# Kernel tuning notes

Measured on AMD Instinct MI355X. Metric: run time of the kernel, lower is better.

The kernel has to match this reference:

```python
import jax, jax.numpy as jnp
import numpy as np

N, IN_F, OUT_F = 4096, 512, 16
HID = [128, 64, 32]
H = 4  # num_head
LRELU_SLOPE = 0.2
BN_EPS = 1e-5
NEG_INF = -1e9


def _gat(x, adj_mask, W, a_src, a_dst, heads, f_out):
    n = x.shape[0]
    h = (x @ W).reshape(n, heads, f_out)              # [N,H,F]
    es = jnp.einsum('nhf,hf->hn', h, a_src)           # [H,N]
    ed = jnp.einsum('nhf,hf->hn', h, a_dst)           # [H,N]
    e = jax.nn.leaky_relu(es[:, :, None] + ed[:, None, :], LRELU_SLOPE)  # [H,N,N]
    e = jnp.where(adj_mask[None], e, NEG_INF)
    attn = jax.nn.softmax(e, axis=-1)                 # masked softmax over neighbors
    out = jnp.einsum('hij,jhf->ihf', attn, h)         # [N,H,F]
    return out.reshape(n, heads * f_out)


def _bn_elu(x, gamma, beta):
    mu = jnp.mean(x, axis=0)
    var = jnp.var(x, axis=0)
    xhat = (x - mu) * jax.lax.rsqrt(var + BN_EPS)
    return jax.nn.elu(xhat * gamma + beta)


def setup_inputs() -> dict:
    key = jax.random.key(0)
    ks = jax.random.split(key, 14)
    s = lambda fin: 1.0 / np.sqrt(fin)
    x = jax.random.normal(ks[0], (N, IN_F), jnp.float32)
    adj = jax.random.randint(ks[1], (N, N), 0, 2, jnp.int32)
    W1 = jax.random.normal(ks[2], (IN_F, H * HID[0]), jnp.float32) * s(IN_F)
    a1s = jax.random.normal(ks[3], (H, HID[0]), jnp.float32) * s(HID[0])
    a1d = jax.random.normal(ks[4], (H, HID[0]), jnp.float32) * s(HID[0])
    lw1 = jax.random.normal(ks[5], (H * HID[0], HID[1]), jnp.float32) * s(H * HID[0])
    lb1 = jnp.zeros((HID[1],), jnp.float32)
    g1 = jnp.ones((HID[1],), jnp.float32)
    be1 = jnp.zeros((HID[1],), jnp.float32)
    W2 = jax.random.normal(ks[6], (HID[1], H * HID[2]), jnp.float32) * s(HID[1])
    a2s = jax.random.normal(ks[7], (H, HID[2]), jnp.float32) * s(HID[2])
    a2d = jax.random.normal(ks[8], (H, HID[2]), jnp.float32) * s(HID[2])
    lw2 = jax.random.normal(ks[9], (H * HID[2], OUT_F), jnp.float32) * s(H * HID[2])
    lb2 = jnp.zeros((OUT_F,), jnp.float32)
    g2 = jnp.ones((OUT_F,), jnp.float32)
    be2 = jnp.zeros((OUT_F,), jnp.float32)
    return dict(x=x, adj=adj, W1=W1, a1s=a1s, a1d=a1d, lw1=lw1, lb1=lb1, g1=g1, be1=be1,
                W2=W2, a2s=a2s, a2d=a2d, lw2=lw2, lb2=lb2, g2=g2, be2=be2)


def reference(x, adj, W1, a1s, a1d, lw1, lb1, g1, be1, W2, a2s, a2d, lw2, lb2, g2, be2):
    adj_mask = adj > 0
    x1 = _gat(x, adj_mask, W1, a1s, a1d, H, HID[0])        # [N, H*128]
    x2 = _bn_elu(x1 @ lw1 + lb1, g1, be1)                  # [N, 64]
    x3 = _gat(x2, adj_mask, W2, a2s, a2d, H, HID[2])       # [N, H*32]
    out = _bn_elu(x3 @ lw2 + lb2, g2, be2)                 # [N, 16]
    return out
```

## Files before the change

kernel.cpp:

```cpp
#include <hip/hip_runtime.h>
#include <hip/hip_bf16.h>
#include <stdint.h>

#define NN 4096
#define H4 4

typedef __hip_bfloat16 bf16;
typedef unsigned short ushort_t;
typedef unsigned long long ull_t;
typedef __attribute__((ext_vector_type(4))) float f32x4;
typedef __attribute__((ext_vector_type(8))) short s16x8;

__device__ __forceinline__ ushort_t f2bf(float f) {
  unsigned u = __float_as_uint(f);
  return (ushort_t)((u + 0x7fff + ((u >> 16) & 1)) >> 16);
}
__device__ __forceinline__ float bf2f(ushort_t h) {
  return __uint_as_float((unsigned)h << 16);
}
__device__ __forceinline__ short2 pkbf(float a, float b) {
  union { __hip_bfloat162 h; short2 s; } u;
  u.h = __float22bfloat162_rn(make_float2(a, b));
  return u.s;
}
__device__ __forceinline__ s16x8 as_s16x8(uint4 v) {
  union { uint4 u; s16x8 s; } c; c.u = v; return c.s;
}

__global__ __launch_bounds__(256) void k_mask(const int* __restrict__ adj,
                                              ull_t* __restrict__ mask) {
  int row = blockIdx.x, tid = threadIdx.x;
  int lane = tid & 63, wv = tid >> 6;
  const int* arow = adj + (size_t)row * NN;
  for (int c = 0; c < NN; c += 256) {
    int col = c + wv * 64 + lane;
    ull_t b = __ballot(arow[col] != 0);
    if (lane == 0) mask[row * 64 + (c >> 6) + wv] = b;
  }
}

__global__ __launch_bounds__(256) void k_gemm(const float* __restrict__ A,
                                              const float* __restrict__ B,
                                              const float* __restrict__ bias,
                                              float* __restrict__ C, int M, int K, int Nc) {
  __shared__ float As[16][68];
  __shared__ float Bs[16][68];
  int tid = threadIdx.x;
  int tx = tid & 15, ty = tid >> 4;
  int mBase = blockIdx.y * 64, nBase = blockIdx.x * 64;
  float acc[4][4] = {};
  for (int k0 = 0; k0 < K; k0 += 16) {
#pragma unroll
    for (int l = 0; l < 4; ++l) {
      int idx = l * 256 + tid;
      int m = idx >> 4, k = idx & 15;
      As[k][m] = A[(size_t)(mBase + m) * K + (k0 + k)];
    }
#pragma unroll
    for (int l = 0; l < 4; ++l) {
      int idx = l * 256 + tid;
      int k = idx >> 6, n = idx & 63;
      int gn = nBase + n;
      Bs[k][n] = (gn < Nc) ? B[(size_t)(k0 + k) * Nc + gn] : 0.f;
    }
    __syncthreads();
#pragma unroll
    for (int k = 0; k < 16; ++k) {
      float4 a = *(const float4*)&As[k][ty * 4];
      float4 b = *(const float4*)&Bs[k][tx * 4];
      float av[4] = {a.x, a.y, a.z, a.w};
      float bv[4] = {b.x, b.y, b.z, b.w};
#pragma unroll
      for (int r = 0; r < 4; ++r)
#pragma unroll
        for (int c = 0; c < 4; ++c) acc[r][c] += av[r] * bv[c];
    }
    __syncthreads();
  }
#pragma unroll
  for (int r = 0; r < 4; ++r) {
    int gm = mBase + ty * 4 + r;
#pragma unroll
    for (int c = 0; c < 4; ++c) {
      int gn = nBase + tx * 4 + c;
      if (gn < Nc) {
        float v = acc[r][c];
        if (bias) v += bias[gn];
        C[(size_t)gm * Nc + gn] = v;
      }
    }
  }
}

#define APLANE (4096 * 512)
template <int KK, int NC>
__device__ __forceinline__ void packW_dev(const float* __restrict__ W,
                                          ushort_t* __restrict__ pk, int tau, int lane) {
  constexpr int KS = KK / 32;
  constexpr int T = (NC / 16) * KS;
  constexpr int PL = T * 512;
  if (tau >= T) return;
  int q = lane >> 4, nn = lane & 15;
  int ct = tau / KS, ks = tau % KS;
  ushort_t hi[8], lo[8];
#pragma unroll
  for (int u = 0; u < 8; ++u) {
    float v = W[(size_t)(ks * 32 + q * 8 + u) * NC + ct * 16 + nn];
    hi[u] = f2bf(v);
    lo[u] = f2bf(v - bf2f(hi[u]));
  }
  size_t idx = ((size_t)(ct * KS + ks) * 64 + lane) * 8;
  *(uint4*)&pk[idx] = *(uint4*)hi;
  *(uint4*)&pk[PL + idx] = *(uint4*)lo;
}

__global__ __launch_bounds__(256) void k_packP(const float* __restrict__ x,
                                               const float* __restrict__ W1,
                                               const float* __restrict__ lw1,
                                               const float* __restrict__ lw2,
                                               ushort_t* __restrict__ pkA,
                                               ushort_t* __restrict__ pkW1,
                                               ushort_t* __restrict__ pkLW1,
                                               ushort_t* __restrict__ pkLW2) {
  int b = blockIdx.x, t = threadIdx.x;
  int w = t >> 6, lane = t & 63;
  if (b < 1024) {
    int q = lane >> 4, nn = lane & 15;
    int tau = b * 4 + w;
    int mt = tau >> 4, ks = tau & 15;
    const float* src = &x[(size_t)(mt * 16 + nn) * 512 + ks * 32 + q * 8];
    float4 v0 = *(const float4*)src;
    float4 v1 = *(const float4*)(src + 4);
    float vv[8] = {v0.x, v0.y, v0.z, v0.w, v1.x, v1.y, v1.z, v1.w};
    ushort_t hi[8], lo[8];
#pragma unroll
    for (int u = 0; u < 8; ++u) {
      hi[u] = f2bf(vv[u]);
      lo[u] = f2bf(vv[u] - bf2f(hi[u]));
    }
    size_t idx = ((size_t)(mt * 16 + ks) * 64 + lane) * 8;
    *(uint4*)&pkA[idx] = *(uint4*)hi;
    *(uint4*)&pkA[APLANE + idx] = *(uint4*)lo;
  } else if (b < 1152) {
    packW_dev<512, 512>(W1, pkW1, (b - 1024) * 4 + w, lane);
  } else if (b < 1168) {
    packW_dev<512, 64>(lw1, pkLW1, (b - 1152) * 4 + w, lane);
  } else {
    packW_dev<128, 16>(lw2, pkLW2, (b - 1168) * 4 + w, lane);
  }
}

__global__ __launch_bounds__(256, 1) void k_mm1(const uint4* __restrict__ pkA,
                                                const uint4* __restrict__ pkW,
                                                float* __restrict__ h1) {
  constexpr int APL4 = APLANE / 8;
  constexpr int WPL4 = (512 / 16) * (512 / 32) * 64;
  int t = threadIdx.x;
  int w = t >> 6, lane = t & 63;
  int q = lane >> 4, nn = lane & 15;
  int mt0 = blockIdx.x * 4 + (w & 1) * 2;
  int ct0 = blockIdx.y * 8 + (w >> 1) * 4;
  f32x4 acc[2][4];
#pragma unroll
  for (int rt = 0; rt < 2; ++rt)
#pragma unroll
    for (int c = 0; c < 4; ++c)
#pragma unroll
      for (int k = 0; k < 4; ++k) acc[rt][c][k] = 0.f;
#pragma unroll
  for (int ks = 0; ks < 16; ++ks) {
    int ia0 = (mt0 * 16 + ks) * 64 + lane;
    int ia1 = ((mt0 + 1) * 16 + ks) * 64 + lane;
    uint4 ah0 = pkA[ia0], ah1 = pkA[ia1];
    uint4 al0 = pkA[APL4 + ia0], al1 = pkA[APL4 + ia1];
    uint4 bh[4], bl[4];
#pragma unroll
    for (int c = 0; c < 4; ++c) {
      int ib = ((ct0 + c) * 16 + ks) * 64 + lane;
      bh[c] = pkW[ib];
      bl[c] = pkW[WPL4 + ib];
    }
#pragma unroll
    for (int c = 0; c < 4; ++c) {
      acc[0][c] = __builtin_amdgcn_mfma_f32_16x16x32_bf16(as_s16x8(ah0), as_s16x8(bh[c]), acc[0][c], 0, 0, 0);
      acc[0][c] = __builtin_amdgcn_mfma_f32_16x16x32_bf16(as_s16x8(ah0), as_s16x8(bl[c]), acc[0][c], 0, 0, 0);
      acc[0][c] = __builtin_amdgcn_mfma_f32_16x16x32_bf16(as_s16x8(al0), as_s16x8(bh[c]), acc[0][c], 0, 0, 0);
      acc[1][c] = __builtin_amdgcn_mfma_f32_16x16x32_bf16(as_s16x8(ah1), as_s16x8(bh[c]), acc[1][c], 0, 0, 0);
      acc[1][c] = __builtin_amdgcn_mfma_f32_16x16x32_bf16(as_s16x8(ah1), as_s16x8(bl[c]), acc[1][c], 0, 0, 0);
      acc[1][c] = __builtin_amdgcn_mfma_f32_16x16x32_bf16(as_s16x8(al1), as_s16x8(bh[c]), acc[1][c], 0, 0, 0);
    }
  }
  int rowB = blockIdx.x * 64 + (w & 1) * 32;
#pragma unroll
  for (int rt = 0; rt < 2; ++rt)
#pragma unroll
    for (int c = 0; c < 4; ++c)
#pragma unroll
      for (int reg = 0; reg < 4; ++reg) {
        int gi = rowB + rt * 16 + q * 4 + reg;
        h1[(size_t)gi * 512 + (ct0 + c) * 16 + nn] = acc[rt][c][reg];
      }
}

template <int F, int TB>
__global__ __launch_bounds__(TB) void k_pack(const float* __restrict__ h,
                                             ushort_t* __restrict__ pk) {
  constexpr int CTW = TB / 64;
  int t = threadIdx.x;
  int lane = t & 63, ctw = t >> 6;
  int q = lane >> 4, nn = lane & 15;
  int ks = blockIdx.x, hd = blockIdx.y;
#pragma unroll
  for (int ct = ctw; ct < F / 16; ct += CTW) {
    ushort_t v[8];
#pragma unroll
    for (int u = 0; u < 8; ++u)
      v[u] = f2bf(h[(size_t)(ks * 32 + q * 8 + u) * (H4 * F) + hd * F + ct * 16 + nn]);
    *(uint4*)&pk[((((size_t)hd * (F / 16) + ct) * (NN / 32) + ks) * 64 + lane) * 8] =
        *(uint4*)v;
  }
}

template <int F>
__global__ __launch_bounds__(256) void k_scores(const float* __restrict__ h,
                                                const float* __restrict__ a_s,
                                                const float* __restrict__ a_d,
                                                float* __restrict__ Tt, float* __restrict__ E1,
                                                float* __restrict__ E2, float* __restrict__ D1,
                                                float* __restrict__ D2) {
  int idx = blockIdx.x * 256 + threadIdx.x;
  if (idx >= NN * H4) return;
  int n = idx >> 2, hd = idx & 3;
  const float* hp = h + (size_t)n * (H4 * F) + hd * F;
  const float* sp = a_s + hd * F;
  const float* dp = a_d + hd * F;
  float ss = 0.f, sd = 0.f;
#pragma unroll 4
  for (int f = 0; f < F; ++f) {
    float v = hp[f];
    ss += v * sp[f];
    sd += v * dp[f];
  }
  ss = fminf(fmaxf(ss, -30.f), 30.f);
  sd = fminf(fmaxf(sd, -30.f), 30.f);
  int o = hd * NN + n;
  Tt[o] = __expf(-ss);
  E1[o] = __expf(ss);
  E2[o] = __expf(0.2f * ss);
  D1[o] = __expf(sd);
  D2[o] = __expf(0.2f * sd);
}

__device__ __forceinline__ s16x8 build_af(float E1i, float E2i, float Ti, unsigned byt,
                                          float4 d1a, float4 d1b, float4 d2a, float4 d2b,
                                          float& rs) {
  float d1[8] = {d1a.x, d1a.y, d1a.z, d1a.w, d1b.x, d1b.y, d1b.z, d1b.w};
  float d2[8] = {d2a.x, d2a.y, d2a.z, d2a.w, d2b.x, d2b.y, d2b.z, d2b.w};
  union { s16x8 v; short2 p[4]; } A;
#pragma unroll
  for (int tp = 0; tp < 4; ++tp) {
    int k0 = 2 * tp, k1 = 2 * tp + 1;
    bool p0 = d1[k0] > Ti;
    float u0 = (p0 ? E1i : E2i) * (p0 ? d1[k0] : d2[k0]);
    u0 = (byt & (1u << k0)) ? u0 : 0.f;
    bool p1 = d1[k1] > Ti;
    float u1 = (p1 ? E1i : E2i) * (p1 ? d1[k1] : d2[k1]);
    u1 = (byt & (1u << k1)) ? u1 : 0.f;
    rs += u0 + u1;
    A.p[tp] = pkbf(u0, u1);
  }
  return A.v;
}

template <int F, int OUTM>
__global__ __launch_bounds__(256, 2) void k_agg_mfma(
    const uint4* __restrict__ pk, const float* __restrict__ Tt,
    const float* __restrict__ E1, const float* __restrict__ E2,
    const float* __restrict__ D1, const float* __restrict__ D2,
    const ull_t* __restrict__ mask, ushort_t* __restrict__ pkOut) {
  constexpr int CT = F / 16;
  constexpr int KSO = (H4 * F) / 32;
  constexpr int OPL = NN * H4 * F;
  __shared__ float red[2 * 32 * F];
  __shared__ float rsred[32 * 4];
  int t = threadIdx.x;
  int w = t >> 6, lane = t & 63;
  int q = lane >> 4, nn = lane & 15;
  int hd = blockIdx.y;
  int rowBase = blockIdx.x * 32;
  int jBase = w * (NN / 4);
  int ia0 = rowBase + nn, ia1 = rowBase + 16 + nn;
  float E1i0 = E1[hd * NN + ia0], E2i0 = E2[hd * NN + ia0], Ti0 = Tt[hd * NN + ia0];
  float E1i1 = E1[hd * NN + ia1], E2i1 = E2[hd * NN + ia1], Ti1 = Tt[hd * NN + ia1];
  const ull_t* mk0p = mask + (size_t)ia0 * 64;
  const ull_t* mk1p = mask + (size_t)ia1 * 64;
  const float* d1h = D1 + hd * NN;
  const float* d2h = D2 + hd * NN;

  f32x4 acc[2][CT];
#pragma unroll
  for (int rt = 0; rt < 2; ++rt)
#pragma unroll
    for (int cc = 0; cc < CT; ++cc)
#pragma unroll
      for (int k = 0; k < 4; ++k) acc[rt][cc][k] = 0.f;
  float rs0 = 0.f, rs1 = 0.f;

  for (int jc = 0; jc < NN / 4 / 64; ++jc) {
    int j0 = jBase + jc * 64;
    int ks0 = j0 >> 5;
    uint4 bv[2][CT];
#pragma unroll
    for (int s = 0; s < 2; ++s)
#pragma unroll
      for (int cc = 0; cc < CT; ++cc)
        bv[s][cc] = pk[(size_t)((hd * CT + cc) * (NN / 32) + ks0 + s) * 64 + lane];
    ull_t mk0 = mk0p[j0 >> 6], mk1 = mk1p[j0 >> 6];
    float4 d1a = *(const float4*)&d1h[j0 + q * 8];
    float4 d1b = *(const float4*)&d1h[j0 + q * 8 + 4];
    float4 d2a = *(const float4*)&d2h[j0 + q * 8];
    float4 d2b = *(const float4*)&d2h[j0 + q * 8 + 4];
    float4 d1c = *(const float4*)&d1h[j0 + 32 + q * 8];
    float4 d1d = *(const float4*)&d1h[j0 + 32 + q * 8 + 4];
    float4 d2c = *(const float4*)&d2h[j0 + 32 + q * 8];
    float4 d2d = *(const float4*)&d2h[j0 + 32 + q * 8 + 4];
    s16x8 a00 = build_af(E1i0, E2i0, Ti0, (unsigned)(mk0 >> (q * 8)) & 0xffu, d1a, d1b, d2a, d2b, rs0);
    s16x8 a01 = build_af(E1i0, E2i0, Ti0, (unsigned)(mk0 >> (32 + q * 8)) & 0xffu, d1c, d1d, d2c, d2d, rs0);
    s16x8 a10 = build_af(E1i1, E2i1, Ti1, (unsigned)(mk1 >> (q * 8)) & 0xffu, d1a, d1b, d2a, d2b, rs1);
    s16x8 a11 = build_af(E1i1, E2i1, Ti1, (unsigned)(mk1 >> (32 + q * 8)) & 0xffu, d1c, d1d, d2c, d2d, rs1);
#pragma unroll
    for (int cc = 0; cc < CT; ++cc)
      acc[0][cc] = __builtin_amdgcn_mfma_f32_16x16x32_bf16(a00, as_s16x8(bv[0][cc]), acc[0][cc], 0, 0, 0);
#pragma unroll
    for (int cc = 0; cc < CT; ++cc)
      acc[0][cc] = __builtin_amdgcn_mfma_f32_16x16x32_bf16(a01, as_s16x8(bv[1][cc]), acc[0][cc], 0, 0, 0);
#pragma unroll
    for (int cc = 0; cc < CT; ++cc)
      acc[1][cc] = __builtin_amdgcn_mfma_f32_16x16x32_bf16(a10, as_s16x8(bv[0][cc]), acc[1][cc], 0, 0, 0);
#pragma unroll
    for (int cc = 0; cc < CT; ++cc)
      acc[1][cc] = __builtin_amdgcn_mfma_f32_16x16x32_bf16(a11, as_s16x8(bv[1][cc]), acc[1][cc], 0, 0, 0);
  }

  rs0 += __shfl_xor(rs0, 16, 64); rs0 += __shfl_xor(rs0, 32, 64);
  rs1 += __shfl_xor(rs1, 16, 64); rs1 += __shfl_xor(rs1, 32, 64);
  if (q == 0) {
    rsred[nn * 4 + w] = rs0;
    rsred[(16 + nn) * 4 + w] = rs1;
  }

#define IDX(rt, cc, reg) ((rt * 16 + q * 4 + reg) * F + cc * 16 + nn)
  if (w == 1 || w == 3) {
    int base = (w >> 1) * 32 * F;
#pragma unroll
    for (int rt = 0; rt < 2; ++rt)
#pragma unroll
      for (int cc = 0; cc < CT; ++cc)
#pragma unroll
        for (int reg = 0; reg < 4; ++reg) red[base + IDX(rt, cc, reg)] = acc[rt][cc][reg];
  }
  __syncthreads();
  if (w == 0 || w == 2) {
    int base = (w >> 1) * 32 * F;
#pragma unroll
    for (int rt = 0; rt < 2; ++rt)
#pragma unroll
      for (int cc = 0; cc < CT; ++cc)
#pragma unroll
        for (int reg = 0; reg < 4; ++reg) acc[rt][cc][reg] += red[base + IDX(rt, cc, reg)];
  }
  if (w == 2) {
#pragma unroll
    for (int rt = 0; rt < 2; ++rt)
#pragma unroll
      for (int cc = 0; cc < CT; ++cc)
#pragma unroll
        for (int reg = 0; reg < 4; ++reg) red[32 * F + IDX(rt, cc, reg)] = acc[rt][cc][reg];
  }
  __syncthreads();
  if (w == 0) {
    float rinv[2][4];
#pragma unroll
    for (int rt = 0; rt < 2; ++rt)
#pragma unroll
      for (int reg = 0; reg < 4; ++reg) {
        int row = rt * 16 + q * 4 + reg;
        float4 rv = *(float4*)&rsred[row * 4];
        float s = (rv.x + rv.y) + (rv.z + rv.w);
        rinv[rt][reg] = (s > 0.f) ? 1.f / s : 0.f;
      }
#pragma unroll
    for (int rt = 0; rt < 2; ++rt)
#pragma unroll
      for (int cc = 0; cc < CT; ++cc)
#pragma unroll
        for (int reg = 0; reg < 4; ++reg) {
          float v = (acc[rt][cc][reg] + red[32 * F + IDX(rt, cc, reg)]) * rinv[rt][reg];
          int gi = rowBase + rt * 16 + q * 4 + reg;
          int c = hd * F + cc * 16 + nn;
          int mt = gi >> 4, rowin = gi & 15;
          int ks = c >> 5, qp = (c >> 3) & 3, u = c & 7;
          size_t idx = (((size_t)mt * KSO + ks) * 64 + qp * 16 + rowin) * 8 + u;
          ushort_t hi = f2bf(v);
          pkOut[idx] = hi;
          if (OUTM == 1) pkOut[OPL + idx] = f2bf(v - bf2f(hi));
        }
  }
#undef IDX
}

__global__ __launch_bounds__(256) void k_mm2(const uint4* __restrict__ pkX,
                                             const uint4* __restrict__ pkW,
                                             const float* __restrict__ bias,
                                             float* __restrict__ y) {
  constexpr int WPL4 = 4 * 16 * 64;
  __shared__ float red[2 * 16 * 64];
  int t = threadIdx.x;
  int w = t >> 6, lane = t & 63;
  int q = lane >> 4, nn = lane & 15;
  int mt = blockIdx.x * 2 + (w & 1);
  int kh = w >> 1;
  f32x4 acc[4];
#pragma unroll
  for (int c = 0; c < 4; ++c)
#pragma unroll
    for (int k = 0; k < 4; ++k) acc[c][k] = 0.f;
#pragma unroll
  for (int k8 = 0; k8 < 8; ++k8) {
    int ks = kh * 8 + k8;
    uint4 a = pkX[(mt * 16 + ks) * 64 + lane];
#pragma unroll
    for (int c = 0; c < 4; ++c) {
      uint4 bh = pkW[(c * 16 + ks) * 64 + lane];
      uint4 bl = pkW[WPL4 + (c * 16 + ks) * 64 + lane];
      acc[c] = __builtin_amdgcn_mfma_f32_16x16x32_bf16(as_s16x8(a), as_s16x8(bh), acc[c], 0, 0, 0);
      acc[c] = __builtin_amdgcn_mfma_f32_16x16x32_bf16(as_s16x8(a), as_s16x8(bl), acc[c], 0, 0, 0);
    }
  }
  int base = (w & 1) * 1024;
  if (kh == 1) {
#pragma unroll
    for (int c = 0; c < 4; ++c)
#pragma unroll
      for (int reg = 0; reg < 4; ++reg)
        red[base + (q * 4 + reg) * 64 + c * 16 + nn] = acc[c][reg];
  }
  __syncthreads();
  if (kh == 0) {
#pragma unroll
    for (int c = 0; c < 4; ++c)
#pragma unroll
      for (int reg = 0; reg < 4; ++reg) {
        float v = acc[c][reg] + red[base + (q * 4 + reg) * 64 + c * 16 + nn] + bias[c * 16 + nn];
        y[(size_t)(mt * 16 + q * 4 + reg) * 64 + c * 16 + nn] = v;
      }
  }
}

__global__ __launch_bounds__(256) void k_mm4(const uint4* __restrict__ pkX,
                                             const uint4* __restrict__ pkW,
                                             const float* __restrict__ bias,
                                             float* __restrict__ y) {
  constexpr int XPL4 = 256 * 4 * 64;
  constexpr int WPL4 = 1 * 4 * 64;
  int t = threadIdx.x;
  int w = t >> 6, lane = t & 63;
  int q = lane >> 4, nn = lane & 15;
  int mt = blockIdx.x * 4 + w;
  f32x4 acc;
#pragma unroll
  for (int k = 0; k < 4; ++k) acc[k] = 0.f;
#pragma unroll
  for (int ks = 0; ks < 4; ++ks) {
    uint4 ah = pkX[(mt * 4 + ks) * 64 + lane];
    uint4 al = pkX[XPL4 + (mt * 4 + ks) * 64 + lane];
    uint4 bh = pkW[ks * 64 + lane];
    uint4 bl = pkW[WPL4 + ks * 64 + lane];
    acc = __builtin_amdgcn_mfma_f32_16x16x32_bf16(as_s16x8(ah), as_s16x8(bh), acc, 0, 0, 0);
    acc = __builtin_amdgcn_mfma_f32_16x16x32_bf16(as_s16x8(ah), as_s16x8(bl), acc, 0, 0, 0);
    acc = __builtin_amdgcn_mfma_f32_16x16x32_bf16(as_s16x8(al), as_s16x8(bh), acc, 0, 0, 0);
  }
  float b = bias[nn];
#pragma unroll
  for (int reg = 0; reg < 4; ++reg)
    y[(size_t)(mt * 16 + q * 4 + reg) * 16 + nn] = acc[reg] + b;
}

__global__ __launch_bounds__(256) void k_bn_col(const float* __restrict__ y,
                                                const float* __restrict__ gamma,
                                                const float* __restrict__ beta,
                                                float* __restrict__ o, int C) {
  int c = blockIdx.x, tid = threadIdx.x;
  float s = 0.f, s2 = 0.f;
  for (int r = tid; r < NN; r += 256) {
    float v = y[(size_t)r * C + c];
    s += v;
    s2 += v * v;
  }
  __shared__ float sh[256], sh2[256];
  __shared__ float smu, srs;
  sh[tid] = s; sh2[tid] = s2;
  __syncthreads();
  for (int off = 128; off; off >>= 1) {
    if (tid < off) { sh[tid] += sh[tid + off]; sh2[tid] += sh2[tid + off]; }
    __syncthreads();
  }
  if (tid == 0) {
    float mu = sh[0] * (1.f / NN);
    float var = sh2[0] * (1.f / NN) - mu * mu;
    smu = mu;
    srs = rsqrtf(fmaxf(var, 0.f) + 1e-5f);
  }
  __syncthreads();
  float mu = smu, rstd = srs, g = gamma[c], b = beta[c];
  for (int r = tid; r < NN; r += 256) {
    float v = (y[(size_t)r * C + c] - mu) * rstd * g + b;
    v = v > 0.f ? v : (__expf(v) - 1.f);
    o[(size_t)r * C + c] = v;
  }
}

extern "C" void kernel_launch(void* const* d_in, const int* in_sizes, int n_in,
                              void* d_out, int out_size, void* d_ws, size_t ws_size,
                              hipStream_t stream) {
  (void)in_sizes; (void)n_in; (void)out_size; (void)ws_size;
  const float* x   = (const float*)d_in[0];
  const int*   adj = (const int*)d_in[1];
  const float* W1  = (const float*)d_in[2];
  const float* a1s = (const float*)d_in[3];
  const float* a1d = (const float*)d_in[4];
  const float* lw1 = (const float*)d_in[5];
  const float* lb1 = (const float*)d_in[6];
  const float* g1  = (const float*)d_in[7];
  const float* be1 = (const float*)d_in[8];
  const float* W2  = (const float*)d_in[9];
  const float* a2s = (const float*)d_in[10];
  const float* a2d = (const float*)d_in[11];
  const float* lw2 = (const float*)d_in[12];
  const float* lb2 = (const float*)d_in[13];
  const float* g2  = (const float*)d_in[14];
  const float* be2 = (const float*)d_in[15];
  float* out = (float*)d_out;

  char* w = (char*)d_ws;
  const size_t MB = 1u << 20;
  ull_t*    mask  = (ull_t*)(w + 0);
  ushort_t* pkA   = (ushort_t*)(w + 2 * MB);
  ushort_t* pkW1  = (ushort_t*)(w + 10 * MB);
  float*    h1    = (float*)(w + 11 * MB);
  ushort_t* pk1   = (ushort_t*)(w + 19 * MB);
  float*    T1    = (float*)(w + 23 * MB);
  float*    E1a   = T1 + 16384;
  float*    E2a   = E1a + 16384;
  float*    D1a   = E2a + 16384;
  float*    D2a   = D1a + 16384;
  ushort_t* pkX1  = (ushort_t*)(w + 24 * MB);
  ushort_t* pkLW1 = (ushort_t*)(w + 28 * MB);
  float*    y1    = (float*)(w + 29 * MB);
  float*    x2    = (float*)(w + 30 * MB);
  float*    h2    = (float*)(w + 31 * MB);
  ushort_t* pk2   = (ushort_t*)(w + 33 * MB);
  float*    T2    = (float*)(w + 34 * MB);
  float*    E1b   = T2 + 16384;
  float*    E2b   = E1b + 16384;
  float*    D1b   = E2b + 16384;
  float*    D2b   = D1b + 16384;
  ushort_t* pkX3  = (ushort_t*)(w + 35 * MB);
  ushort_t* pkLW2 = (ushort_t*)(w + 37 * MB);
  float*    y2    = (float*)(w + 37 * MB + 131072);

  k_mask<<<NN, 256, 0, stream>>>(adj, mask);
  k_packP<<<1169, 256, 0, stream>>>(x, W1, lw1, lw2, pkA, pkW1, pkLW1, pkLW2);

  k_mm1<<<dim3(64, 4), 256, 0, stream>>>((const uint4*)pkA, (const uint4*)pkW1, h1);
  k_pack<128, 256><<<dim3(NN / 32, H4), 256, 0, stream>>>(h1, pk1);
  k_scores<128><<<(NN * H4) / 256, 256, 0, stream>>>(h1, a1s, a1d, T1, E1a, E2a, D1a, D2a);
  k_agg_mfma<128, 0><<<dim3(NN / 32, H4), 256, 0, stream>>>((const uint4*)pk1, T1, E1a, E2a,
                                                            D1a, D2a, mask, pkX1);

  k_mm2<<<128, 256, 0, stream>>>((const uint4*)pkX1, (const uint4*)pkLW1, lb1, y1);
  k_bn_col<<<64, 256, 0, stream>>>(y1, g1, be1, x2, 64);

  k_gemm<<<dim3(2, 64), 256, 0, stream>>>(x2, W2, nullptr, h2, NN, 64, 128);
  k_pack<32, 128><<<dim3(NN / 32, H4), 128, 0, stream>>>(h2, pk2);
  k_scores<32><<<(NN * H4) / 256, 256, 0, stream>>>(h2, a2s, a2d, T2, E1b, E2b, D1b, D2b);
  k_agg_mfma<32, 1><<<dim3(NN / 32, H4), 256, 0, stream>>>((const uint4*)pk2, T2, E1b, E2b,
                                                           D1b, D2b, mask, pkX3);

  k_mm4<<<64, 256, 0, stream>>>((const uint4*)pkX3, (const uint4*)pkLW2, lb2, y2);
  k_bn_col<<<16, 256, 0, stream>>>(y2, g2, be2, out, 16);
}
```

Baseline: 294.0 us.

## Build attention weights in packed fp16 and fold row sums into MFMA

Score exponentials are stored as scaled fp16, and attention weights are formed with packed fp16 multiply and max (max(E1*D1, E2*D2) is exp of the leaky relu), replacing the per-element compare and select in fp32. Row sums come from an extra MFMA against a ones vector instead of scalar accumulation and shuffles. The aggregation MFMAs switch from bf16 to fp16 and the reduction buffer is padded. The intent is to cut VALU work in the attention build loop. In exchange, scores are clamped to ±8 and fp16 range and precision limits could affect accuracy.

```diff
diff --git a/kernel.cpp b/kernel.cpp
--- a/kernel.cpp
+++ b/kernel.cpp
@@ -10,6 +10,8 @@
 typedef unsigned long long ull_t;
 typedef __attribute__((ext_vector_type(4))) float f32x4;
 typedef __attribute__((ext_vector_type(8))) short s16x8;
+typedef __attribute__((ext_vector_type(2))) _Float16 h16x2;
+typedef __attribute__((ext_vector_type(8))) _Float16 h16x8;
 
 __device__ __forceinline__ ushort_t f2bf(float f) {
   unsigned u = __float_as_uint(f);
@@ -18,13 +20,25 @@
 __device__ __forceinline__ float bf2f(ushort_t h) {
   return __uint_as_float((unsigned)h << 16);
 }
-__device__ __forceinline__ short2 pkbf(float a, float b) {
-  union { __hip_bfloat162 h; short2 s; } u;
-  u.h = __float22bfloat162_rn(make_float2(a, b));
-  return u.s;
-}
 __device__ __forceinline__ s16x8 as_s16x8(uint4 v) {
   union { uint4 u; s16x8 s; } c; c.u = v; return c.s;
+}
+__device__ __forceinline__ unsigned pkmul(unsigned a, unsigned b) {
+  union { unsigned u; h16x2 v; } A, B, R;
+  A.u = a; B.u = b;
+  R.v = A.v * B.v;
+  return R.u;
+}
+__device__ __forceinline__ unsigned pkmax(unsigned a, unsigned b) {
+  union { unsigned u; h16x2 v; } A, B, R;
+  A.u = a; B.u = b;
+  R.v = __builtin_elementwise_max(A.v, B.v);
+  return R.u;
+}
+__device__ __forceinline__ ushort_t f2h(float f) {
+  union { _Float16 h; ushort_t s; } c;
+  c.h = (_Float16)f;
+  return c.s;
 }
 
 __global__ __launch_bounds__(256) void k_mask(const int* __restrict__ adj,
@@ -215,7 +229,7 @@
     ushort_t v[8];
 #pragma unroll
     for (int u = 0; u < 8; ++u)
-      v[u] = f2bf(h[(size_t)(ks * 32 + q * 8 + u) * (H4 * F) + hd * F + ct * 16 + nn]);
+      v[u] = f2h(h[(size_t)(ks * 32 + q * 8 + u) * (H4 * F) + hd * F + ct * 16 + nn]);
     *(uint4*)&pk[((((size_t)hd * (F / 16) + ct) * (NN / 32) + ks) * 64 + lane) * 8] =
         *(uint4*)v;
   }
@@ -225,9 +239,10 @@
 __global__ __launch_bounds__(256) void k_scores(const float* __restrict__ h,
                                                 const float* __restrict__ a_s,
                                                 const float* __restrict__ a_d,
-                                                float* __restrict__ Tt, float* __restrict__ E1,
-                                                float* __restrict__ E2, float* __restrict__ D1,
-                                                float* __restrict__ D2) {
+                                                ushort_t* __restrict__ E1s,
+                                                ushort_t* __restrict__ E2s,
+                                                ushort_t* __restrict__ D1s,
+                                                ushort_t* __restrict__ D2s) {
   int idx = blockIdx.x * 256 + threadIdx.x;
   if (idx >= NN * H4) return;
   int n = idx >> 2, hd = idx & 3;
@@ -241,48 +256,44 @@
     ss += v * sp[f];
     sd += v * dp[f];
   }
-  ss = fminf(fmaxf(ss, -30.f), 30.f);
-  sd = fminf(fmaxf(sd, -30.f), 30.f);
+  ss = fminf(fmaxf(ss, -8.f), 8.f);
+  sd = fminf(fmaxf(sd, -8.f), 8.f);
   int o = hd * NN + n;
-  Tt[o] = __expf(-ss);
-  E1[o] = __expf(ss);
-  E2[o] = __expf(0.2f * ss);
-  D1[o] = __expf(sd);
-  D2[o] = __expf(0.2f * sd);
-}
-
-__device__ __forceinline__ s16x8 build_af(float E1i, float E2i, float Ti, unsigned byt,
-                                          float4 d1a, float4 d1b, float4 d2a, float4 d2b,
-                                          float& rs) {
-  float d1[8] = {d1a.x, d1a.y, d1a.z, d1a.w, d1b.x, d1b.y, d1b.z, d1b.w};
-  float d2[8] = {d2a.x, d2a.y, d2a.z, d2a.w, d2b.x, d2b.y, d2b.z, d2b.w};
-  union { s16x8 v; short2 p[4]; } A;
+  E1s[o] = f2h(__expf(ss) * 0.0625f);
+  E2s[o] = f2h(__expf(0.2f * ss) * 0.0625f);
+  D1s[o] = f2h(__expf(sd) * 0.0625f);
+  D2s[o] = f2h(__expf(0.2f * sd) * 0.0625f);
+}
+
+__device__ __forceinline__ void build_af(unsigned E1pk, unsigned E2pk, unsigned byt,
+                                         uint4 d1, uint4 d2, unsigned out[4]) {
+  unsigned d1v[4] = {d1.x, d1.y, d1.z, d1.w};
+  unsigned d2v[4] = {d2.x, d2.y, d2.z, d2.w};
 #pragma unroll
   for (int tp = 0; tp < 4; ++tp) {
-    int k0 = 2 * tp, k1 = 2 * tp + 1;
-    bool p0 = d1[k0] > Ti;
-    float u0 = (p0 ? E1i : E2i) * (p0 ? d1[k0] : d2[k0]);
-    u0 = (byt & (1u << k0)) ? u0 : 0.f;
-    bool p1 = d1[k1] > Ti;
-    float u1 = (p1 ? E1i : E2i) * (p1 ? d1[k1] : d2[k1]);
-    u1 = (byt & (1u << k1)) ? u1 : 0.f;
-    rs += u0 + u1;
-    A.p[tp] = pkbf(u0, u1);
-  }
-  return A.v;
+    unsigned u = pkmax(pkmul(E1pk, d1v[tp]), pkmul(E2pk, d2v[tp]));
+    int mlo = (int)(byt << (31 - 2 * tp)) >> 31;
+    int mhi = (int)(byt << (30 - 2 * tp)) >> 31;
+    out[tp] = u & (((unsigned)mlo & 0xFFFFu) | ((unsigned)mhi << 16));
+  }
+}
+__device__ __forceinline__ h16x8 as_h16x8(const unsigned w[4]) {
+  union { unsigned u[4]; h16x8 v; } c;
+  c.u[0] = w[0]; c.u[1] = w[1]; c.u[2] = w[2]; c.u[3] = w[3];
+  return c.v;
 }
 
 template <int F, int OUTM>
 __global__ __launch_bounds__(256, 2) void k_agg_mfma(
-    const uint4* __restrict__ pk, const float* __restrict__ Tt,
-    const float* __restrict__ E1, const float* __restrict__ E2,
-    const float* __restrict__ D1, const float* __restrict__ D2,
-    const ull_t* __restrict__ mask, ushort_t* __restrict__ pkOut) {
+    const uint4* __restrict__ pk, const ushort_t* __restrict__ E1s,
+    const ushort_t* __restrict__ E2s, const ushort_t* __restrict__ D1s,
+    const ushort_t* __restrict__ D2s, const ull_t* __restrict__ mask,
+    ushort_t* __restrict__ pkOut) {
   constexpr int CT = F / 16;
+  constexpr int RW = F + 16;
   constexpr int KSO = (H4 * F) / 32;
   constexpr int OPL = NN * H4 * F;
-  __shared__ float red[2 * 32 * F];
-  __shared__ float rsred[32 * 4];
+  __shared__ float red[2 * 32 * RW];
   int t = threadIdx.x;
   int w = t >> 6, lane = t & 63;
   int q = lane >> 4, nn = lane & 15;
@@ -290,22 +301,28 @@
   int rowBase = blockIdx.x * 32;
   int jBase = w * (NN / 4);
   int ia0 = rowBase + nn, ia1 = rowBase + 16 + nn;
-  float E1i0 = E1[hd * NN + ia0], E2i0 = E2[hd * NN + ia0], Ti0 = Tt[hd * NN + ia0];
-  float E1i1 = E1[hd * NN + ia1], E2i1 = E2[hd * NN + ia1], Ti1 = Tt[hd * NN + ia1];
+  unsigned E1p0 = (unsigned)E1s[hd * NN + ia0] * 0x00010001u;
+  unsigned E2p0 = (unsigned)E2s[hd * NN + ia0] * 0x00010001u;
+  unsigned E1p1 = (unsigned)E1s[hd * NN + ia1] * 0x00010001u;
+  unsigned E2p1 = (unsigned)E2s[hd * NN + ia1] * 0x00010001u;
   const ull_t* mk0p = mask + (size_t)ia0 * 64;
   const ull_t* mk1p = mask + (size_t)ia1 * 64;
-  const float* d1h = D1 + hd * NN;
-  const float* d2h = D2 + hd * NN;
-
-  f32x4 acc[2][CT];
+  const ushort_t* d1h = D1s + hd * NN;
+  const ushort_t* d2h = D2s + hd * NN;
+
+  h16x8 ones;
+#pragma unroll
+  for (int k = 0; k < 8; ++k) ones[k] = (_Float16)1.0f;
+
+  f32x4 acc[2][CT + 1];
 #pragma unroll
   for (int rt = 0; rt < 2; ++rt)
 #pragma unroll
-    for (int cc = 0; cc < CT; ++cc)
+    for (int cc = 0; cc <= CT; ++cc)
 #pragma unroll
       for (int k = 0; k < 4; ++k) acc[rt][cc][k] = 0.f;
-  float rs0 = 0.f, rs1 = 0.f;
-
+
+#pragma unroll 2
   for (int jc = 0; jc < NN / 4 / 64; ++jc) {
     int j0 = jBase + jc * 64;
     int ks0 = j0 >> 5;
@@ -316,56 +333,49 @@
       for (int cc = 0; cc < CT; ++cc)
         bv[s][cc] = pk[(size_t)((hd * CT + cc) * (NN / 32) + ks0 + s) * 64 + lane];
     ull_t mk0 = mk0p[j0 >> 6], mk1 = mk1p[j0 >> 6];
-    float4 d1a = *(const float4*)&d1h[j0 + q * 8];
-    float4 d1b = *(const float4*)&d1h[j0 + q * 8 + 4];
-    float4 d2a = *(const float4*)&d2h[j0 + q * 8];
-    float4 d2b = *(const float4*)&d2h[j0 + q * 8 + 4];
-    float4 d1c = *(const float4*)&d1h[j0 + 32 + q * 8];
-    float4 d1d = *(const float4*)&d1h[j0 + 32 + q * 8 + 4];
-    float4 d2c = *(const float4*)&d2h[j0 + 32 + q * 8];
-    float4 d2d = *(const float4*)&d2h[j0 + 32 + q * 8 + 4];
-    s16x8 a00 = build_af(E1i0, E2i0, Ti0, (unsigned)(mk0 >> (q * 8)) & 0xffu, d1a, d1b, d2a, d2b, rs0);
-    s16x8 a01 = build_af(E1i0, E2i0, Ti0, (unsigned)(mk0 >> (32 + q * 8)) & 0xffu, d1c, d1d, d2c, d2d, rs0);
-    s16x8 a10 = build_af(E1i1, E2i1, Ti1, (unsigned)(mk1 >> (q * 8)) & 0xffu, d1a, d1b, d2a, d2b, rs1);
-    s16x8 a11 = build_af(E1i1, E2i1, Ti1, (unsigned)(mk1 >> (32 + q * 8)) & 0xffu, d1c, d1d, d2c, d2d, rs1);
-#pragma unroll
-    for (int cc = 0; cc < CT; ++cc)
-      acc[0][cc] = __builtin_amdgcn_mfma_f32_16x16x32_bf16(a00, as_s16x8(bv[0][cc]), acc[0][cc], 0, 0, 0);
-#pragma unroll
-    for (int cc = 0; cc < CT; ++cc)
-      acc[0][cc] = __builtin_amdgcn_mfma_f32_16x16x32_bf16(a01, as_s16x8(bv[1][cc]), acc[0][cc], 0, 0, 0);
-#pragma unroll
-    for (int cc = 0; cc < CT; ++cc)
-      acc[1][cc] = __builtin_amdgcn_mfma_f32_16x16x32_bf16(a10, as_s16x8(bv[0][cc]), acc[1][cc], 0, 0, 0);
-#pragma unroll
-    for (int cc = 0; cc < CT; ++cc)
-      acc[1][cc] = __builtin_amdgcn_mfma_f32_16x16x32_bf16(a11, as_s16x8(bv[1][cc]), acc[1][cc], 0, 0, 0);
-  }
-
-  rs0 += __shfl_xor(rs0, 16, 64); rs0 += __shfl_xor(rs0, 32, 64);
-  rs1 += __shfl_xor(rs1, 16, 64); rs1 += __shfl_xor(rs1, 32, 64);
-  if (q == 0) {
-    rsred[nn * 4 + w] = rs0;
-    rsred[(16 + nn) * 4 + w] = rs1;
-  }
-
-#define IDX(rt, cc, reg) ((rt * 16 + q * 4 + reg) * F + cc * 16 + nn)
+    uint4 d1a = *(const uint4*)&d1h[j0 + q * 8];
+    uint4 d2a = *(const uint4*)&d2h[j0 + q * 8];
+    uint4 d1b = *(const uint4*)&d1h[j0 + 32 + q * 8];
+    uint4 d2b = *(const uint4*)&d2h[j0 + 32 + q * 8];
+    unsigned a00[4], a01[4], a10[4], a11[4];
+    build_af(E1p0, E2p0, (unsigned)(mk0 >> (q * 8)) & 0xffu, d1a, d2a, a00);
+    build_af(E1p0, E2p0, (unsigned)(mk0 >> (32 + q * 8)) & 0xffu, d1b, d2b, a01);
+    build_af(E1p1, E2p1, (unsigned)(mk1 >> (q * 8)) & 0xffu, d1a, d2a, a10);
+    build_af(E1p1, E2p1, (unsigned)(mk1 >> (32 + q * 8)) & 0xffu, d1b, d2b, a11);
+    h16x8 A00 = as_h16x8(a00), A01 = as_h16x8(a01);
+    h16x8 A10 = as_h16x8(a10), A11 = as_h16x8(a11);
+#pragma unroll
+    for (int cc = 0; cc < CT; ++cc) {
+      union { uint4 u; h16x8 v; } b0, b1;
+      b0.u = bv[0][cc]; b1.u = bv[1][cc];
+      acc[0][cc] = __builtin_amdgcn_mfma_f32_16x16x32_f16(A00, b0.v, acc[0][cc], 0, 0, 0);
+      acc[0][cc] = __builtin_amdgcn_mfma_f32_16x16x32_f16(A01, b1.v, acc[0][cc], 0, 0, 0);
+      acc[1][cc] = __builtin_amdgcn_mfma_f32_16x16x32_f16(A10, b0.v, acc[1][cc], 0, 0, 0);
+      acc[1][cc] = __builtin_amdgcn_mfma_f32_16x16x32_f16(A11, b1.v, acc[1][cc], 0, 0, 0);
+    }
+    acc[0][CT] = __builtin_amdgcn_mfma_f32_16x16x32_f16(A00, ones, acc[0][CT], 0, 0, 0);
+    acc[0][CT] = __builtin_amdgcn_mfma_f32_16x16x32_f16(A01, ones, acc[0][CT], 0, 0, 0);
+    acc[1][CT] = __builtin_amdgcn_mfma_f32_16x16x32_f16(A10, ones, acc[1][CT], 0, 0, 0);
+    acc[1][CT] = __builtin_amdgcn_mfma_f32_16x16x32_f16(A11, ones, acc[1][CT], 0, 0, 0);
+  }
+
+#define IDX(rt, cc, reg) ((rt * 16 + q * 4 + reg) * RW + cc * 16 + nn)
   if (w == 1 || w == 3) {
-    int base = (w >> 1) * 32 * F;
+    int base = (w >> 1) * 32 * RW;
 #pragma unroll
     for (int rt = 0; rt < 2; ++rt)
 #pragma unroll
-      for (int cc = 0; cc < CT; ++cc)
+      for (int cc = 0; cc <= CT; ++cc)
 #pragma unroll
         for (int reg = 0; reg < 4; ++reg) red[base + IDX(rt, cc, reg)] = acc[rt][cc][reg];
   }
   __syncthreads();
   if (w == 0 || w == 2) {
-    int base = (w >> 1) * 32 * F;
+    int base = (w >> 1) * 32 * RW;
 #pragma unroll
     for (int rt = 0; rt < 2; ++rt)
 #pragma unroll
-      for (int cc = 0; cc < CT; ++cc)
+      for (int cc = 0; cc <= CT; ++cc)
 #pragma unroll
         for (int reg = 0; reg < 4; ++reg) acc[rt][cc][reg] += red[base + IDX(rt, cc, reg)];
   }
@@ -373,9 +383,9 @@
 #pragma unroll
     for (int rt = 0; rt < 2; ++rt)
 #pragma unroll
-      for (int cc = 0; cc < CT; ++cc)
-#pragma unroll
-        for (int reg = 0; reg < 4; ++reg) red[32 * F + IDX(rt, cc, reg)] = acc[rt][cc][reg];
+      for (int cc = 0; cc <= CT; ++cc)
+#pragma unroll
+        for (int reg = 0; reg < 4; ++reg) red[32 * RW + IDX(rt, cc, reg)] = acc[rt][cc][reg];
   }
   __syncthreads();
   if (w == 0) {
@@ -384,9 +394,7 @@
     for (int rt = 0; rt < 2; ++rt)
 #pragma unroll
       for (int reg = 0; reg < 4; ++reg) {
-        int row = rt * 16 + q * 4 + reg;
-        float4 rv = *(float4*)&rsred[row * 4];
-        float s = (rv.x + rv.y) + (rv.z + rv.w);
+        float s = acc[rt][CT][reg] + red[32 * RW + IDX(rt, CT, reg)];
         rinv[rt][reg] = (s > 0.f) ? 1.f / s : 0.f;
       }
 #pragma unroll
@@ -395,7 +403,7 @@
       for (int cc = 0; cc < CT; ++cc)
 #pragma unroll
         for (int reg = 0; reg < 4; ++reg) {
-          float v = (acc[rt][cc][reg] + red[32 * F + IDX(rt, cc, reg)]) * rinv[rt][reg];
+          float v = (acc[rt][cc][reg] + red[32 * RW + IDX(rt, cc, reg)]) * rinv[rt][reg];
           int gi = rowBase + rt * 16 + q * 4 + reg;
           int c = hd * F + cc * 16 + nn;
           int mt = gi >> 4, rowin = gi & 15;
@@ -549,22 +557,20 @@
   ushort_t* pkW1  = (ushort_t*)(w + 10 * MB);
   float*    h1    = (float*)(w + 11 * MB);
   ushort_t* pk1   = (ushort_t*)(w + 19 * MB);
-  float*    T1    = (float*)(w + 23 * MB);
-  float*    E1a   = T1 + 16384;
-  float*    E2a   = E1a + 16384;
-  float*    D1a   = E2a + 16384;
-  float*    D2a   = D1a + 16384;
+  ushort_t* E1a   = (ushort_t*)(w + 23 * MB);
+  ushort_t* E2a   = E1a + 16384;
+  ushort_t* D1a   = E2a + 16384;
+  ushort_t* D2a   = D1a + 16384;
   ushort_t* pkX1  = (ushort_t*)(w + 24 * MB);
   ushort_t* pkLW1 = (ushort_t*)(w + 28 * MB);
   float*    y1    = (float*)(w + 29 * MB);
   float*    x2    = (float*)(w + 30 * MB);
   float*    h2    = (float*)(w + 31 * MB);
   ushort_t* pk2   = (ushort_t*)(w + 33 * MB);
-  float*    T2    = (float*)(w + 34 * MB);
-  float*    E1b   = T2 + 16384;
-  float*    E2b   = E1b + 16384;
-  float*    D1b   = E2b + 16384;
-  float*    D2b   = D1b + 16384;
+  ushort_t* E1b   = (ushort_t*)(w + 34 * MB);
+  ushort_t* E2b   = E1b + 16384;
+  ushort_t* D1b   = E2b + 16384;
+  ushort_t* D2b   = D1b + 16384;
   ushort_t* pkX3  = (ushort_t*)(w + 35 * MB);
   ushort_t* pkLW2 = (ushort_t*)(w + 37 * MB);
   float*    y2    = (float*)(w + 37 * MB + 131072);
@@ -574,8 +580,8 @@
 
   k_mm1<<<dim3(64, 4), 256, 0, stream>>>((const uint4*)pkA, (const uint4*)pkW1, h1);
   k_pack<128, 256><<<dim3(NN / 32, H4), 256, 0, stream>>>(h1, pk1);
-  k_scores<128><<<(NN * H4) / 256, 256, 0, stream>>>(h1, a1s, a1d, T1, E1a, E2a, D1a, D2a);
-  k_agg_mfma<128, 0><<<dim3(NN / 32, H4), 256, 0, stream>>>((const uint4*)pk1, T1, E1a, E2a,
+  k_scores<128><<<(NN * H4) / 256, 256, 0, stream>>>(h1, a1s, a1d, E1a, E2a, D1a, D2a);
+  k_agg_mfma<128, 0><<<dim3(NN / 32, H4), 256, 0, stream>>>((const uint4*)pk1, E1a, E2a,
                                                             D1a, D2a, mask, pkX1);
 
   k_mm2<<<128, 256, 0, stream>>>((const uint4*)pkX1, (const uint4*)pkLW1, lb1, y1);
@@ -583,8 +589,8 @@
 
   k_gemm<<<dim3(2, 64), 256, 0, stream>>>(x2, W2, nullptr, h2, NN, 64, 128);
   k_pack<32, 128><<<dim3(NN / 32, H4), 128, 0, stream>>>(h2, pk2);
-  k_scores<32><<<(NN * H4) / 256, 256, 0, stream>>>(h2, a2s, a2d, T2, E1b, E2b, D1b, D2b);
-  k_agg_mfma<32, 1><<<dim3(NN / 32, H4), 256, 0, stream>>>((const uint4*)pk2, T2, E1b, E2b,
+  k_scores<32><<<(NN * H4) / 256, 256, 0, stream>>>(h2, a2s, a2d, E1b, E2b, D1b, D2b);
+  k_agg_mfma<32, 1><<<dim3(NN / 32, H4), 256, 0, stream>>>((const uint4*)pk2, E1b, E2b,
                                                            D1b, D2b, mask, pkX3);
 
   k_mm4<<<64, 256, 0, stream>>>((const uint4*)pkX3, (const uint4*)pkLW2, lb2, y2);
```

Result: slower. 331.9 us (+12.9%).

## Split attention aggregation across eight waves per block with two-stage reduction

Applied to the files above, without the earlier changes.

Doubles the attention-aggregation block size from 4 to 8 wavefronts, so each wave covers one eighth of the neighbour range instead of a quarter. The cross-wave partial sums now go through a two-level LDS reduction tree with an extra barrier, plus a wider row-sum table. The goal is more in-flight waves per block to hide memory and MFMA latency on a grid of only 512 blocks. In exchange it needs more LDS for partial results and an extra synchronisation. The tighter launch bound (512 threads, 4 blocks) may squeeze the register budget enough to force spills in the F=128 instance.

```diff
diff --git a/kernel.cpp b/kernel.cpp
--- a/kernel.cpp
+++ b/kernel.cpp
@@ -273,7 +273,7 @@
 }
 
 template <int F, int OUTM>
-__global__ __launch_bounds__(256, 2) void k_agg_mfma(
+__global__ __launch_bounds__(512, 4) void k_agg_mfma(
     const uint4* __restrict__ pk, const float* __restrict__ Tt,
     const float* __restrict__ E1, const float* __restrict__ E2,
     const float* __restrict__ D1, const float* __restrict__ D2,
@@ -281,14 +281,15 @@
   constexpr int CT = F / 16;
   constexpr int KSO = (H4 * F) / 32;
   constexpr int OPL = NN * H4 * F;
-  __shared__ float red[2 * 32 * F];
-  __shared__ float rsred[32 * 4];
+  constexpr int REG = 32 * F;
+  __shared__ float red[4 * REG];
+  __shared__ float rsred[32 * 8];
   int t = threadIdx.x;
   int w = t >> 6, lane = t & 63;
   int q = lane >> 4, nn = lane & 15;
   int hd = blockIdx.y;
   int rowBase = blockIdx.x * 32;
-  int jBase = w * (NN / 4);
+  int jBase = w * (NN / 8);
   int ia0 = rowBase + nn, ia1 = rowBase + 16 + nn;
   float E1i0 = E1[hd * NN + ia0], E2i0 = E2[hd * NN + ia0], Ti0 = Tt[hd * NN + ia0];
   float E1i1 = E1[hd * NN + ia1], E2i1 = E2[hd * NN + ia1], Ti1 = Tt[hd * NN + ia1];
@@ -306,7 +307,7 @@
       for (int k = 0; k < 4; ++k) acc[rt][cc][k] = 0.f;
   float rs0 = 0.f, rs1 = 0.f;
 
-  for (int jc = 0; jc < NN / 4 / 64; ++jc) {
+  for (int jc = 0; jc < NN / 8 / 64; ++jc) {
     int j0 = jBase + jc * 64;
     int ks0 = j0 >> 5;
     uint4 bv[2][CT];
@@ -345,13 +346,13 @@
   rs0 += __shfl_xor(rs0, 16, 64); rs0 += __shfl_xor(rs0, 32, 64);
   rs1 += __shfl_xor(rs1, 16, 64); rs1 += __shfl_xor(rs1, 32, 64);
   if (q == 0) {
-    rsred[nn * 4 + w] = rs0;
-    rsred[(16 + nn) * 4 + w] = rs1;
+    rsred[nn * 8 + w] = rs0;
+    rsred[(16 + nn) * 8 + w] = rs1;
   }
 
 #define IDX(rt, cc, reg) ((rt * 16 + q * 4 + reg) * F + cc * 16 + nn)
-  if (w == 1 || w == 3) {
-    int base = (w >> 1) * 32 * F;
+  if (w >= 4) {
+    int base = (w - 4) * REG;
 #pragma unroll
     for (int rt = 0; rt < 2; ++rt)
 #pragma unroll
@@ -360,8 +361,8 @@
         for (int reg = 0; reg < 4; ++reg) red[base + IDX(rt, cc, reg)] = acc[rt][cc][reg];
   }
   __syncthreads();
-  if (w == 0 || w == 2) {
-    int base = (w >> 1) * 32 * F;
+  if (w < 4) {
+    int base = w * REG;
 #pragma unroll
     for (int rt = 0; rt < 2; ++rt)
 #pragma unroll
@@ -369,13 +370,32 @@
 #pragma unroll
         for (int reg = 0; reg < 4; ++reg) acc[rt][cc][reg] += red[base + IDX(rt, cc, reg)];
   }
-  if (w == 2) {
+  if (w == 2 || w == 3) {
+    int base = w * REG;
 #pragma unroll
     for (int rt = 0; rt < 2; ++rt)
 #pragma unroll
       for (int cc = 0; cc < CT; ++cc)
 #pragma unroll
-        for (int reg = 0; reg < 4; ++reg) red[32 * F + IDX(rt, cc, reg)] = acc[rt][cc][reg];
+        for (int reg = 0; reg < 4; ++reg) red[base + IDX(rt, cc, reg)] = acc[rt][cc][reg];
+  }
+  __syncthreads();
+  if (w == 0 || w == 1) {
+    int base = (w + 2) * REG;
+#pragma unroll
+    for (int rt = 0; rt < 2; ++rt)
+#pragma unroll
+      for (int cc = 0; cc < CT; ++cc)
+#pragma unroll
+        for (int reg = 0; reg < 4; ++reg) acc[rt][cc][reg] += red[base + IDX(rt, cc, reg)];
+  }
+  if (w == 1) {
+#pragma unroll
+    for (int rt = 0; rt < 2; ++rt)
+#pragma unroll
+      for (int cc = 0; cc < CT; ++cc)
+#pragma unroll
+        for (int reg = 0; reg < 4; ++reg) red[REG + IDX(rt, cc, reg)] = acc[rt][cc][reg];
   }
   __syncthreads();
   if (w == 0) {
@@ -385,8 +405,9 @@
 #pragma unroll
       for (int reg = 0; reg < 4; ++reg) {
         int row = rt * 16 + q * 4 + reg;
-        float4 rv = *(float4*)&rsred[row * 4];
-        float s = (rv.x + rv.y) + (rv.z + rv.w);
+        float4 ra = *(float4*)&rsred[row * 8];
+        float4 rb = *(float4*)&rsred[row * 8 + 4];
+        float s = ((ra.x + ra.y) + (ra.z + ra.w)) + ((rb.x + rb.y) + (rb.z + rb.w));
         rinv[rt][reg] = (s > 0.f) ? 1.f / s : 0.f;
       }
 #pragma unroll
@@ -395,7 +416,7 @@
       for (int cc = 0; cc < CT; ++cc)
 #pragma unroll
         for (int reg = 0; reg < 4; ++reg) {
-          float v = (acc[rt][cc][reg] + red[32 * F + IDX(rt, cc, reg)]) * rinv[rt][reg];
+          float v = (acc[rt][cc][reg] + red[REG + IDX(rt, cc, reg)]) * rinv[rt][reg];
           int gi = rowBase + rt * 16 + q * 4 + reg;
           int c = hd * F + cc * 16 + nn;
           int mt = gi >> 4, rowin = gi & 15;
@@ -575,7 +596,7 @@
   k_mm1<<<dim3(64, 4), 256, 0, stream>>>((const uint4*)pkA, (const uint4*)pkW1, h1);
   k_pack<128, 256><<<dim3(NN / 32, H4), 256, 0, stream>>>(h1, pk1);
   k_scores<128><<<(NN * H4) / 256, 256, 0, stream>>>(h1, a1s, a1d, T1, E1a, E2a, D1a, D2a);
-  k_agg_mfma<128, 0><<<dim3(NN / 32, H4), 256, 0, stream>>>((const uint4*)pk1, T1, E1a, E2a,
+  k_agg_mfma<128, 0><<<dim3(NN / 32, H4), 512, 0, stream>>>((const uint4*)pk1, T1, E1a, E2a,
                                                             D1a, D2a, mask, pkX1);
 
   k_mm2<<<128, 256, 0, stream>>>((const uint4*)pkX1, (const uint4*)pkLW1, lb1, y1);
@@ -584,7 +605,7 @@
   k_gemm<<<dim3(2, 64), 256, 0, stream>>>(x2, W2, nullptr, h2, NN, 64, 128);
   k_pack<32, 128><<<dim3(NN / 32, H4), 128, 0, stream>>>(h2, pk2);
   k_scores<32><<<(NN * H4) / 256, 256, 0, stream>>>(h2, a2s, a2d, T2, E1b, E2b, D1b, D2b);
-  k_agg_mfma<32, 1><<<dim3(NN / 32, H4), 256, 0, stream>>>((const uint4*)pk2, T2, E1b, E2b,
+  k_agg_mfma<32, 1><<<dim3(NN / 32, H4), 512, 0, stream>>>((const uint4*)pk2, T2, E1b, E2b,
                                                            D1b, D2b, mask, pkX3);
 
   k_mm4<<<64, 256, 0, stream>>>((const uint4*)pkX3, (const uint4*)pkLW2, lb2, y2);
```

After: 523.1 us. +77.9%, slower.

## Split GAT aggregation over neighbor halves with separate combine kernel

Applied to the files above, without the earlier changes.

The attention-aggregation kernel now splits the neighbor (j) dimension into two halves across separate blocks, doubling the grid from 512 to 1024 blocks. Each block writes unnormalized fp32 partial sums and row sums to scratch buffers. A new combine kernel adds the two partials, normalizes, and writes the packed bf16 output. This is meant to raise parallelism and occupancy on the many-CU GPU, at the cost of extra global traffic for the fp32 partials (about 16MB for layer 1) and two extra kernel launches.

```diff
diff --git a/kernel.cpp b/kernel.cpp
--- a/kernel.cpp
+++ b/kernel.cpp
@@ -272,23 +272,23 @@
   return A.v;
 }
 
-template <int F, int OUTM>
+template <int F>
 __global__ __launch_bounds__(256, 2) void k_agg_mfma(
     const uint4* __restrict__ pk, const float* __restrict__ Tt,
     const float* __restrict__ E1, const float* __restrict__ E2,
     const float* __restrict__ D1, const float* __restrict__ D2,
-    const ull_t* __restrict__ mask, ushort_t* __restrict__ pkOut) {
+    const ull_t* __restrict__ mask, float* __restrict__ Pp, float* __restrict__ rsp) {
   constexpr int CT = F / 16;
-  constexpr int KSO = (H4 * F) / 32;
-  constexpr int OPL = NN * H4 * F;
+  constexpr int PL = NN * H4 * F;
   __shared__ float red[2 * 32 * F];
   __shared__ float rsred[32 * 4];
   int t = threadIdx.x;
   int w = t >> 6, lane = t & 63;
   int q = lane >> 4, nn = lane & 15;
   int hd = blockIdx.y;
-  int rowBase = blockIdx.x * 32;
-  int jBase = w * (NN / 4);
+  int rowBase = (blockIdx.x >> 1) * 32;
+  int half = blockIdx.x & 1;
+  int jBase = half * (NN / 2) + w * (NN / 8);
   int ia0 = rowBase + nn, ia1 = rowBase + 16 + nn;
   float E1i0 = E1[hd * NN + ia0], E2i0 = E2[hd * NN + ia0], Ti0 = Tt[hd * NN + ia0];
   float E1i1 = E1[hd * NN + ia1], E2i1 = E2[hd * NN + ia1], Ti1 = Tt[hd * NN + ia1];
@@ -306,7 +306,7 @@
       for (int k = 0; k < 4; ++k) acc[rt][cc][k] = 0.f;
   float rs0 = 0.f, rs1 = 0.f;
 
-  for (int jc = 0; jc < NN / 4 / 64; ++jc) {
+  for (int jc = 0; jc < NN / 8 / 64; ++jc) {
     int j0 = jBase + jc * 64;
     int ks0 = j0 >> 5;
     uint4 bv[2][CT];
@@ -379,34 +379,48 @@
   }
   __syncthreads();
   if (w == 0) {
-    float rinv[2][4];
+    float* Pb = Pp + (size_t)half * PL + (size_t)(hd * NN) * F;
 #pragma unroll
     for (int rt = 0; rt < 2; ++rt)
 #pragma unroll
       for (int reg = 0; reg < 4; ++reg) {
         int row = rt * 16 + q * 4 + reg;
-        float4 rv = *(float4*)&rsred[row * 4];
-        float s = (rv.x + rv.y) + (rv.z + rv.w);
-        rinv[rt][reg] = (s > 0.f) ? 1.f / s : 0.f;
+        int gi = rowBase + row;
+        if (nn == 0) {
+          float4 rv = *(float4*)&rsred[row * 4];
+          rsp[(size_t)half * H4 * NN + hd * NN + gi] = (rv.x + rv.y) + (rv.z + rv.w);
+        }
+#pragma unroll
+        for (int cc = 0; cc < CT; ++cc)
+          Pb[(size_t)gi * F + cc * 16 + nn] =
+              acc[rt][cc][reg] + red[32 * F + IDX(rt, cc, reg)];
       }
-#pragma unroll
-    for (int rt = 0; rt < 2; ++rt)
-#pragma unroll
-      for (int cc = 0; cc < CT; ++cc)
-#pragma unroll
-        for (int reg = 0; reg < 4; ++reg) {
-          float v = (acc[rt][cc][reg] + red[32 * F + IDX(rt, cc, reg)]) * rinv[rt][reg];
-          int gi = rowBase + rt * 16 + q * 4 + reg;
-          int c = hd * F + cc * 16 + nn;
-          int mt = gi >> 4, rowin = gi & 15;
-          int ks = c >> 5, qp = (c >> 3) & 3, u = c & 7;
-          size_t idx = (((size_t)mt * KSO + ks) * 64 + qp * 16 + rowin) * 8 + u;
-          ushort_t hi = f2bf(v);
-          pkOut[idx] = hi;
-          if (OUTM == 1) pkOut[OPL + idx] = f2bf(v - bf2f(hi));
-        }
   }
 #undef IDX
+}
+
+template <int F, int OUTM>
+__global__ __launch_bounds__(256) void k_combine(const float* __restrict__ P,
+                                                 const float* __restrict__ rs,
+                                                 ushort_t* __restrict__ pkOut) {
+  constexpr int PL = NN * H4 * F;
+  constexpr int KSO = (H4 * F) / 32;
+  constexpr int OPL = NN * H4 * F;
+  int idx = blockIdx.x * 256 + threadIdx.x;
+  int f = idx % F;
+  int rem = idx / F;
+  int i = rem % NN;
+  int hd = rem / NN;
+  float p = P[idx] + P[PL + idx];
+  float s = rs[hd * NN + i] + rs[H4 * NN + hd * NN + i];
+  float v = p * ((s > 0.f) ? 1.f / s : 0.f);
+  int c = hd * F + f;
+  int mt = i >> 4, rowin = i & 15;
+  int ks = c >> 5, qp = (c >> 3) & 3, u = c & 7;
+  size_t o = (((size_t)mt * KSO + ks) * 64 + qp * 16 + rowin) * 8 + u;
+  ushort_t hi = f2bf(v);
+  pkOut[o] = hi;
+  if (OUTM == 1) pkOut[OPL + o] = f2bf(v - bf2f(hi));
 }
 
 __global__ __launch_bounds__(256) void k_mm2(const uint4* __restrict__ pkX,
@@ -568,6 +582,10 @@
   ushort_t* pkX3  = (ushort_t*)(w + 35 * MB);
   ushort_t* pkLW2 = (ushort_t*)(w + 37 * MB);
   float*    y2    = (float*)(w + 37 * MB + 131072);
+  float*    P1b   = (float*)(w + 38 * MB);
+  float*    rs1b  = (float*)(w + 54 * MB);
+  float*    P2b   = (float*)(w + 55 * MB);
+  float*    rs2b  = (float*)(w + 59 * MB);
 
   k_mask<<<NN, 256, 0, stream>>>(adj, mask);
   k_packP<<<1169, 256, 0, stream>>>(x, W1, lw1, lw2, pkA, pkW1, pkLW1, pkLW2);
@@ -575,8 +593,9 @@
   k_mm1<<<dim3(64, 4), 256, 0, stream>>>((const uint4*)pkA, (const uint4*)pkW1, h1);
   k_pack<128, 256><<<dim3(NN / 32, H4), 256, 0, stream>>>(h1, pk1);
   k_scores<128><<<(NN * H4) / 256, 256, 0, stream>>>(h1, a1s, a1d, T1, E1a, E2a, D1a, D2a);
-  k_agg_mfma<128, 0><<<dim3(NN / 32, H4), 256, 0, stream>>>((const uint4*)pk1, T1, E1a, E2a,
-                                                            D1a, D2a, mask, pkX1);
+  k_agg_mfma<128><<<dim3(NN / 16, H4), 256, 0, stream>>>((const uint4*)pk1, T1, E1a, E2a,
+                                                         D1a, D2a, mask, P1b, rs1b);
+  k_combine<128, 0><<<(NN * H4 * 128) / 256, 256, 0, stream>>>(P1b, rs1b, pkX1);
 
   k_mm2<<<128, 256, 0, stream>>>((const uint4*)pkX1, (const uint4*)pkLW1, lb1, y1);
   k_bn_col<<<64, 256, 0, stream>>>(y1, g1, be1, x2, 64);
@@ -584,8 +603,9 @@
   k_gemm<<<dim3(2, 64), 256, 0, stream>>>(x2, W2, nullptr, h2, NN, 64, 128);
   k_pack<32, 128><<<dim3(NN / 32, H4), 128, 0, stream>>>(h2, pk2);
   k_scores<32><<<(NN * H4) / 256, 256, 0, stream>>>(h2, a2s, a2d, T2, E1b, E2b, D1b, D2b);
-  k_agg_mfma<32, 1><<<dim3(NN / 32, H4), 256, 0, stream>>>((const uint4*)pk2, T2, E1b, E2b,
-                                                           D1b, D2b, mask, pkX3);
+  k_agg_mfma<32><<<dim3(NN / 16, H4), 256, 0, stream>>>((const uint4*)pk2, T2, E1b, E2b,
+                                                        D1b, D2b, mask, P2b, rs2b);
+  k_combine<32, 1><<<(NN * H4 * 32) / 256, 256, 0, stream>>>(P2b, rs2b, pkX3);
 
   k_mm4<<<64, 256, 0, stream>>>((const uint4*)pkX3, (const uint4*)pkLW2, lb2, y2);
   k_bn_col<<<16, 256, 0, stream>>>(y2, g2, be2, out, 16);
```

Result: slower. 310.3 us (+5.5%).
